# Kernel tuning notes

Measured on AMD Instinct MI355X. Metric: run time of the kernel, lower is better.

## Reference

```python
import jax, jax.numpy as jnp
import numpy as np

D_MODEL = 1024
N_HEADS = 16
HEAD_DIM = D_MODEL // N_HEADS  # 64; used only as softmax scale in windowed path
WINDOW = 128


def _window_starts(seq_len, window):
    # Faithful to the torch loop: stride = window//2, last window right-aligned.
    starts = []
    for i in range(0, seq_len, window // 2):
        end = min(i + window, seq_len)
        starts.append(max(0, end - window))
        if end == seq_len:
            break
    return np.asarray(starts, dtype=np.int32)


def setup_inputs() -> dict:
    key = jax.random.key(0)
    ks = jax.random.split(key, 9)
    B, S = 4, 4096
    sc = 1.0 / np.sqrt(D_MODEL)
    return {
        "x": jax.random.normal(ks[0], (B, S, D_MODEL), jnp.float32),
        "Wq": jax.random.normal(ks[1], (D_MODEL, D_MODEL), jnp.float32) * sc,
        "bq": jax.random.normal(ks[2], (D_MODEL,), jnp.float32) * 0.02,
        "Wk": jax.random.normal(ks[3], (D_MODEL, D_MODEL), jnp.float32) * sc,
        "bk": jax.random.normal(ks[4], (D_MODEL,), jnp.float32) * 0.02,
        "Wv": jax.random.normal(ks[5], (D_MODEL, D_MODEL), jnp.float32) * sc,
        "bv": jax.random.normal(ks[6], (D_MODEL,), jnp.float32) * 0.02,
        "Wo": jax.random.normal(ks[7], (D_MODEL, D_MODEL), jnp.float32) * sc,
        "bo": jax.random.normal(ks[8], (D_MODEL,), jnp.float32) * 0.02,
    }


def reference(x, Wq, bq, Wk, bk, Wv, bv, Wo, bo):
    B, S, D = x.shape
    q = x @ Wq + bq  # [B,S,D]
    k = x @ Wk + bk
    v = x @ Wv + bv

    # Overlapping sliding windows (heads merged, as in the original windowed path).
    starts = _window_starts(S, WINDOW)                      # [W]
    idx = starts[:, None] + np.arange(WINDOW)[None, :]      # [W, w] static
    idx_j = jnp.asarray(idx)
    qw = q[:, idx_j]  # [B, W, w, D]
    kw = k[:, idx_j]
    vw = v[:, idx_j]
    scores = jnp.einsum('bwqd,bwkd->bwqk', qw, kw) / np.sqrt(HEAD_DIM)
    attn = jax.nn.softmax(scores, axis=-1)
    out_w = jnp.einsum('bwqk,bwkd->bwqd', attn, vw)         # [B, W, w, D]

    # Overlap-add then average by coverage counts.
    flat_idx = idx.reshape(-1)
    out = jnp.zeros((B, S, D), x.dtype).at[:, flat_idx].add(
        out_w.reshape(B, -1, D))
    counts = jnp.zeros((S,), x.dtype).at[flat_idx].add(1.0)
    out = out / counts[None, :, None]

    return out @ Wo + bo
```

## Files before the change

kernel.cpp:

```cpp
#include <hip/hip_runtime.h>
#include <stdint.h>
#include <stddef.h>

#define D_MODEL 1024
#define SEQ     4096
#define BATCH   4
#define MTOT    (BATCH*SEQ)
#define NWIN    63

typedef __bf16 bf16;
typedef __bf16 bf16x8 __attribute__((ext_vector_type(8)));
typedef __bf16 bf16x4 __attribute__((ext_vector_type(4)));
typedef float  floatx4 __attribute__((ext_vector_type(4)));

__device__ __forceinline__ void async_ld16(const void* g, void* l) {
  __builtin_amdgcn_global_load_lds(
      (const __attribute__((address_space(1))) unsigned int*)g,
      (__attribute__((address_space(3))) unsigned int*)l,
      16, 0, 0);
}


__global__ __launch_bounds__(256)
void cvt_x_kernel(const float* __restrict__ x, bf16* __restrict__ xb)
{
  const int i = blockIdx.x * 256 + threadIdx.x;
  const float4 v = ((const float4*)x)[i];
  bf16x4 o = { (bf16)v.x, (bf16)v.y, (bf16)v.z, (bf16)v.w };
  ((bf16x4*)xb)[i] = o;
}

__global__ __launch_bounds__(256)
void cvt_wt_kernel(const float* __restrict__ W0, const float* __restrict__ W1,
                   const float* __restrict__ W2, const float* __restrict__ W3,
                   bf16* __restrict__ wt)
{
  __shared__ float tile[32][33];
  const float* Wsel = (blockIdx.z == 0) ? W0 : (blockIdx.z == 1) ? W1
                    : (blockIdx.z == 2) ? W2 : W3;
  bf16* Wt = wt + (size_t)blockIdx.z * D_MODEL * D_MODEL;
  const int tx = threadIdx.x & 31, ty = threadIdx.x >> 5;
  const int tn = blockIdx.x * 32, tk = blockIdx.y * 32;
#pragma unroll
  for (int j = 0; j < 32; j += 8)
    tile[ty + j][tx] = Wsel[(size_t)(tk + ty + j) * D_MODEL + (tn + tx)];
  __syncthreads();
#pragma unroll
  for (int j = 0; j < 32; j += 8)
    Wt[(size_t)(tn + ty + j) * D_MODEL + (tk + tx)] = (bf16)tile[tx][ty + j];
}

__device__ __forceinline__ void gemm_core(const bf16* __restrict__ A,
                                          const bf16* __restrict__ Bt,
                                          int Kdim, int m0, int n0,
                                          bf16* As, bf16* Bs,
                                          floatx4 (&acc)[4][4],
                                          int w, int l)
{
  const int ll = l & 15, lh = l >> 4;
  const int wm = w >> 1, wn = w & 1;

  for (int k0 = 0; k0 < Kdim; k0 += 64) {
#pragma unroll
    for (int i = 0; i < 4; ++i) {
      const int f = w * 4 + i;
      const int mt = f & 7, kk = f >> 3;
      async_ld16(A  + (size_t)(m0 + mt * 16 + ll) * Kdim + (k0 + kk * 32 + lh * 8),
                 &As[f * 512 + l * 8]);
      async_ld16(Bt + (size_t)(n0 + mt * 16 + ll) * Kdim + (k0 + kk * 32 + lh * 8),
                 &Bs[f * 512 + l * 8]);
    }
    __syncthreads();
#pragma unroll
    for (int kk = 0; kk < 2; ++kk) {
      bf16x8 af[4], bfr[4];
#pragma unroll
      for (int t = 0; t < 4; ++t) {
        af[t]  = *(const bf16x8*)&As[(kk * 8 + wm * 4 + t) * 512 + l * 8];
        bfr[t] = *(const bf16x8*)&Bs[(kk * 8 + wn * 4 + t) * 512 + l * 8];
      }
#pragma unroll
      for (int mt = 0; mt < 4; ++mt)
#pragma unroll
        for (int nt = 0; nt < 4; ++nt)
          acc[mt][nt] = __builtin_amdgcn_mfma_f32_16x16x32_bf16(af[mt], bfr[nt], acc[mt][nt], 0, 0, 0);
    }
    __syncthreads();
  }
}

__global__ __launch_bounds__(256)
void gemm_qkv(const bf16* __restrict__ A, const bf16* __restrict__ Bt,
              const float* __restrict__ bq, const float* __restrict__ bk,
              const float* __restrict__ bv,
              bf16* __restrict__ qo, bf16* __restrict__ ko, bf16* __restrict__ vto)
{
  __shared__ __attribute__((aligned(16))) bf16 As[8192];
  __shared__ __attribute__((aligned(16))) bf16 Bs[8192];
  const int tid = threadIdx.x;
  const int w = tid >> 6, l = tid & 63;
  const int ll = l & 15, lh = l >> 4;
  const int wm = w >> 1, wn = w & 1;

  const int idx = blockIdx.x;
  const int xcd = idx & 7;
  const int local = idx >> 3;
  const int msub = local & 3;
  const int nblk = (local >> 2) % 24;
  const int sub  = local / 96;
  const int mblk = xcd * 16 + sub * 4 + msub;
  const int m0 = mblk * 128, n0 = nblk * 128;

  floatx4 acc[4][4];
#pragma unroll
  for (int i = 0; i < 4; ++i)
#pragma unroll
    for (int j = 0; j < 4; ++j) acc[i][j] = (floatx4)0.f;

  gemm_core(A, Bt, D_MODEL, m0, n0, As, Bs, acc, w, l);

  const int sel = n0 >> 10;
  const int ncl = n0 & 1023;
  const float* bias = (sel == 0) ? bq : (sel == 1) ? bk : bv;

#pragma unroll
  for (int mt = 0; mt < 4; ++mt) {
#pragma unroll
    for (int nt = 0; nt < 4; ++nt) {
      const int colL = ncl + wn * 64 + nt * 16 + ll;
      const float bvv = bias[colL];
#pragma unroll
      for (int r = 0; r < 4; ++r) {
        const int row = m0 + wm * 64 + mt * 16 + lh * 4 + r;
        const float v = acc[mt][nt][r] + bvv;
        if (sel == 0) {
          qo[(size_t)row * D_MODEL + colL] = (bf16)v;
        } else if (sel == 1) {
          ko[(size_t)row * D_MODEL + colL] = (bf16)v;
        } else {
          const int bb = row >> 12, s = row & 4095;
          vto[((size_t)bb * D_MODEL + colL) * SEQ + s] = (bf16)v;
        }
      }
    }
  }
}

__global__ __launch_bounds__(256)
void gemm_out(const bf16* __restrict__ A, const bf16* __restrict__ Bt,
              const float* __restrict__ bias, float* __restrict__ C)
{
  __shared__ __attribute__((aligned(16))) bf16 As[8192];
  __shared__ __attribute__((aligned(16))) bf16 Bs[8192];
  const int tid = threadIdx.x;
  const int w = tid >> 6, l = tid & 63;
  const int ll = l & 15, lh = l >> 4;
  const int wm = w >> 1, wn = w & 1;

  const int idx = blockIdx.x;
  const int xcd = idx & 7;
  const int local = idx >> 3;
  const int msub = local & 3;
  const int nblk = (local >> 2) & 7;
  const int sub  = local >> 5;
  const int mblk = xcd * 16 + sub * 4 + msub;
  const int m0 = mblk * 128, n0 = nblk * 128;

  floatx4 acc[4][4];
#pragma unroll
  for (int i = 0; i < 4; ++i)
#pragma unroll
    for (int j = 0; j < 4; ++j) acc[i][j] = (floatx4)0.f;

  gemm_core(A, Bt, D_MODEL, m0, n0, As, Bs, acc, w, l);

#pragma unroll
  for (int mt = 0; mt < 4; ++mt) {
#pragma unroll
    for (int nt = 0; nt < 4; ++nt) {
      const int col = n0 + wn * 64 + nt * 16 + ll;
      const float bvv = bias[col];
#pragma unroll
      for (int r = 0; r < 4; ++r) {
        const int row = m0 + wm * 64 + mt * 16 + lh * 4 + r;
        C[(size_t)row * D_MODEL + col] = acc[mt][nt][r] + bvv;
      }
    }
  }
}

__global__ __launch_bounds__(256)
void qk_softmax(const bf16* __restrict__ qb, const bf16* __restrict__ kb,
                bf16* __restrict__ Pg)
{
  __shared__ __attribute__((aligned(16))) bf16 As[4096];
  __shared__ __attribute__((aligned(16))) bf16 Bs[8192];
  __shared__ float redM[4][64];
  __shared__ float redS[4][64];

  const int tid = threadIdx.x;
  const int w = tid >> 6, l = tid & 63, ll = l & 15, lh = l >> 4;
  const int wh = blockIdx.x;
  const int win = wh >> 1, half = wh & 1;
  const int b = blockIdx.y;

  const bf16* Aq = qb + ((size_t)b * SEQ + win * 64 + half * 64) * D_MODEL;
  const bf16* Ak = kb + ((size_t)b * SEQ + win * 64) * D_MODEL;

  floatx4 acc[4][2];
#pragma unroll
  for (int i = 0; i < 4; ++i)
#pragma unroll
    for (int j = 0; j < 2; ++j) acc[i][j] = (floatx4)0.f;

  for (int c0 = 0; c0 < D_MODEL; c0 += 64) {
#pragma unroll
    for (int i = 0; i < 2; ++i) {
      const int f = w * 2 + i;
      const int mt = f & 3, kk = f >> 2;
      async_ld16(Aq + (size_t)(mt * 16 + ll) * D_MODEL + (c0 + kk * 32 + lh * 8),
                 &As[f * 512 + l * 8]);
    }
#pragma unroll
    for (int i = 0; i < 4; ++i) {
      const int f = w * 4 + i;
      const int mt = f & 7, kk = f >> 3;
      async_ld16(Ak + (size_t)(mt * 16 + ll) * D_MODEL + (c0 + kk * 32 + lh * 8),
                 &Bs[f * 512 + l * 8]);
    }
    __syncthreads();
#pragma unroll
    for (int kk = 0; kk < 2; ++kk) {
      bf16x8 af[4], bfr[2];
#pragma unroll
      for (int t = 0; t < 4; ++t)
        af[t]  = *(const bf16x8*)&As[(kk * 4 + t) * 512 + l * 8];
#pragma unroll
      for (int t = 0; t < 2; ++t)
        bfr[t] = *(const bf16x8*)&Bs[(kk * 8 + w * 2 + t) * 512 + l * 8];
#pragma unroll
      for (int mt = 0; mt < 4; ++mt)
#pragma unroll
        for (int nt = 0; nt < 2; ++nt)
          acc[mt][nt] = __builtin_amdgcn_mfma_f32_16x16x32_bf16(af[mt], bfr[nt], acc[mt][nt], 0, 0, 0);
    }
    __syncthreads();
  }

#pragma unroll
  for (int mt = 0; mt < 4; ++mt)
#pragma unroll
    for (int nt = 0; nt < 2; ++nt)
#pragma unroll
      for (int r = 0; r < 4; ++r) acc[mt][nt][r] *= 0.125f;

#pragma unroll
  for (int mt = 0; mt < 4; ++mt)
#pragma unroll
    for (int r = 0; r < 4; ++r) {
      float m = fmaxf(acc[mt][0][r], acc[mt][1][r]);
      m = fmaxf(m, __shfl_xor(m, 1));
      m = fmaxf(m, __shfl_xor(m, 2));
      m = fmaxf(m, __shfl_xor(m, 4));
      m = fmaxf(m, __shfl_xor(m, 8));
      if (ll == 0) redM[w][mt * 16 + lh * 4 + r] = m;
    }
  __syncthreads();

#pragma unroll
  for (int mt = 0; mt < 4; ++mt)
#pragma unroll
    for (int r = 0; r < 4; ++r) {
      const int row = mt * 16 + lh * 4 + r;
      const float m = fmaxf(fmaxf(redM[0][row], redM[1][row]),
                            fmaxf(redM[2][row], redM[3][row]));
      const float e0 = __expf(acc[mt][0][r] - m);
      const float e1 = __expf(acc[mt][1][r] - m);
      acc[mt][0][r] = e0; acc[mt][1][r] = e1;
      float s = e0 + e1;
      s += __shfl_xor(s, 1);
      s += __shfl_xor(s, 2);
      s += __shfl_xor(s, 4);
      s += __shfl_xor(s, 8);
      if (ll == 0) redS[w][row] = s;
    }
  __syncthreads();

  bf16* Pb = Pg + ((size_t)(b * NWIN + win) * 128 + half * 64) * 128;
#pragma unroll
  for (int mt = 0; mt < 4; ++mt)
#pragma unroll
    for (int r = 0; r < 4; ++r) {
      const int row = mt * 16 + lh * 4 + r;
      const float inv = 1.f / (redS[0][row] + redS[1][row] + redS[2][row] + redS[3][row]);
#pragma unroll
      for (int nt = 0; nt < 2; ++nt)
        Pb[(size_t)row * 128 + w * 32 + nt * 16 + ll] = (bf16)(acc[mt][nt][r] * inv);
    }
}

__global__ __launch_bounds__(256)
void pv_gather(const bf16* __restrict__ Pg, const bf16* __restrict__ vt,
               bf16* __restrict__ ab)
{
  __shared__ __attribute__((aligned(16))) bf16 As[4096];
  __shared__ __attribute__((aligned(16))) bf16 Bs[8192];

  const int tid = threadIdx.x;
  const int w = tid >> 6, l = tid & 63, ll = l & 15, lh = l >> 4;
  const int d0 = blockIdx.x * 128;
  const int h  = blockIdx.y;
  const int b  = blockIdx.z;

  int wseg[2], roff[2];
  int nseg = 0;
  if (h >= 1)        { wseg[nseg] = h - 1; roff[nseg] = 64; ++nseg; }
  if (h <= NWIN - 1) { wseg[nseg] = h;     roff[nseg] = 0;  ++nseg; }
  const float scale = (nseg == 2) ? 0.5f : 1.0f;

  floatx4 acc[4][2];
#pragma unroll
  for (int i = 0; i < 4; ++i)
#pragma unroll
    for (int j = 0; j < 2; ++j) acc[i][j] = (floatx4)0.f;

  for (int sg = 0; sg < nseg; ++sg) {
    const bf16* Pseg = Pg + ((size_t)(b * NWIN + wseg[sg]) * 128 + roff[sg]) * 128;
    const bf16* Vseg = vt + ((size_t)b * D_MODEL + d0) * SEQ + wseg[sg] * 64;
    for (int c0 = 0; c0 < 128; c0 += 64) {
#pragma unroll
      for (int i = 0; i < 2; ++i) {
        const int f = w * 2 + i;
        const int mt = f & 3, kk = f >> 2;
        async_ld16(Pseg + (size_t)(mt * 16 + ll) * 128 + (c0 + kk * 32 + lh * 8),
                   &As[f * 512 + l * 8]);
      }
#pragma unroll
      for (int i = 0; i < 4; ++i) {
        const int f = w * 4 + i;
        const int mt = f & 7, kk = f >> 3;
        async_ld16(Vseg + (size_t)(mt * 16 + ll) * SEQ + (c0 + kk * 32 + lh * 8),
                   &Bs[f * 512 + l * 8]);
      }
      __syncthreads();
#pragma unroll
      for (int kk = 0; kk < 2; ++kk) {
        bf16x8 af[4], bfr[2];
#pragma unroll
        for (int t = 0; t < 4; ++t)
          af[t]  = *(const bf16x8*)&As[(kk * 4 + t) * 512 + l * 8];
#pragma unroll
        for (int t = 0; t < 2; ++t)
          bfr[t] = *(const bf16x8*)&Bs[(kk * 8 + w * 2 + t) * 512 + l * 8];
#pragma unroll
        for (int mt = 0; mt < 4; ++mt)
#pragma unroll
          for (int nt = 0; nt < 2; ++nt)
            acc[mt][nt] = __builtin_amdgcn_mfma_f32_16x16x32_bf16(af[mt], bfr[nt], acc[mt][nt], 0, 0, 0);
      }
      __syncthreads();
    }
  }

#pragma unroll
  for (int mt = 0; mt < 4; ++mt)
#pragma unroll
    for (int nt = 0; nt < 2; ++nt)
#pragma unroll
      for (int r = 0; r < 4; ++r) {
        const int row = h * 64 + mt * 16 + lh * 4 + r;
        const int col = d0 + w * 32 + nt * 16 + ll;
        ab[((size_t)b * SEQ + row) * D_MODEL + col] = (bf16)(acc[mt][nt][r] * scale);
      }
}

extern "C" void kernel_launch(void* const* d_in, const int* in_sizes, int n_in,
                              void* d_out, int out_size, void* d_ws, size_t ws_size,
                              hipStream_t stream)
{
  (void)in_sizes; (void)n_in; (void)out_size;

  const float* x  = (const float*)d_in[0];
  const float* Wq = (const float*)d_in[1];
  const float* bq = (const float*)d_in[2];
  const float* Wk = (const float*)d_in[3];
  const float* bk = (const float*)d_in[4];
  const float* Wv = (const float*)d_in[5];
  const float* bv = (const float*)d_in[6];
  const float* Wo = (const float*)d_in[7];
  const float* bo = (const float*)d_in[8];

  if (ws_size < (size_t)176160768) return;
  char* ws = (char*)d_ws;
  bf16* xb = (bf16*)(ws);
  bf16* pb = (bf16*)(ws);
  bf16* wt = (bf16*)(ws + 33554432);
  bf16* qb = (bf16*)(ws + 41943040);
  bf16* kb = (bf16*)(ws + 75497472);
  bf16* vt = (bf16*)(ws + 109051904);
  bf16* ab = (bf16*)(ws + 142606336);

  cvt_x_kernel<<<16384, 256, 0, stream>>>(x, xb);
  cvt_wt_kernel<<<dim3(32, 32, 4), 256, 0, stream>>>(Wq, Wk, Wv, Wo, wt);

  gemm_qkv<<<3072, 256, 0, stream>>>(xb, wt, bq, bk, bv, qb, kb, vt);

  qk_softmax<<<dim3(126, BATCH), 256, 0, stream>>>(qb, kb, pb);
  pv_gather<<<dim3(8, 64, BATCH), 256, 0, stream>>>(pb, vt, ab);

  gemm_out<<<1024, 256, 0, stream>>>(ab, wt + 3145728, bo, (float*)d_out);
}
```

Before: 497.9 us.

## Double-buffer LDS tiles with register prefetch in GEMM and QK kernels

Replaces the async global-to-LDS loads plus per-iteration sync with a software pipeline. The next K-tile is loaded into registers while MFMAs run on the current LDS buffer, then stored into the alternate buffer. This hides global-load latency behind compute in the QKV, output projection and QK-softmax kernels. In exchange it doubles LDS usage (64KB per block for the GEMMs) and adds register pressure, which may reduce occupancy.

```diff
diff --git a/kernel.cpp b/kernel.cpp
--- a/kernel.cpp
+++ b/kernel.cpp
@@ -50,34 +50,54 @@
     Wt[(size_t)(tn + ty + j) * D_MODEL + (tk + tx)] = (bf16)tile[tx][ty + j];
 }
 
-__device__ __forceinline__ void gemm_core(const bf16* __restrict__ A,
-                                          const bf16* __restrict__ Bt,
-                                          int Kdim, int m0, int n0,
-                                          bf16* As, bf16* Bs,
-                                          floatx4 (&acc)[4][4],
-                                          int w, int l)
+__device__ __forceinline__ void gemm_core_pipe(const bf16* __restrict__ A,
+                                               const bf16* __restrict__ Bt,
+                                               int Kdim, int m0, int n0,
+                                               bf16* As, bf16* Bs,
+                                               floatx4 (&acc)[4][4],
+                                               int w, int l)
 {
   const int ll = l & 15, lh = l >> 4;
   const int wm = w >> 1, wn = w & 1;
 
-  for (int k0 = 0; k0 < Kdim; k0 += 64) {
+  bf16x8 ar[4], br[4];
+
+  auto load_regs = [&](int k0) {
 #pragma unroll
     for (int i = 0; i < 4; ++i) {
       const int f = w * 4 + i;
       const int mt = f & 7, kk = f >> 3;
-      async_ld16(A  + (size_t)(m0 + mt * 16 + ll) * Kdim + (k0 + kk * 32 + lh * 8),
-                 &As[f * 512 + l * 8]);
-      async_ld16(Bt + (size_t)(n0 + mt * 16 + ll) * Kdim + (k0 + kk * 32 + lh * 8),
-                 &Bs[f * 512 + l * 8]);
-    }
-    __syncthreads();
+      ar[i] = *(const bf16x8*)(A  + (size_t)(m0 + mt * 16 + ll) * Kdim + (k0 + kk * 32 + lh * 8));
+      br[i] = *(const bf16x8*)(Bt + (size_t)(n0 + mt * 16 + ll) * Kdim + (k0 + kk * 32 + lh * 8));
+    }
+  };
+  auto store_lds = [&](int buf) {
+    bf16* Ad = As + buf * 8192;
+    bf16* Bd = Bs + buf * 8192;
+#pragma unroll
+    for (int i = 0; i < 4; ++i) {
+      const int f = w * 4 + i;
+      *(bf16x8*)&Ad[f * 512 + l * 8] = ar[i];
+      *(bf16x8*)&Bd[f * 512 + l * 8] = br[i];
+    }
+  };
+
+  load_regs(0);
+  store_lds(0);
+  __syncthreads();
+
+  const int T = Kdim >> 6;
+  for (int t = 0; t < T; ++t) {
+    if (t + 1 < T) load_regs((t + 1) << 6);
+    const bf16* Ac = As + (t & 1) * 8192;
+    const bf16* Bc = Bs + (t & 1) * 8192;
 #pragma unroll
     for (int kk = 0; kk < 2; ++kk) {
       bf16x8 af[4], bfr[4];
 #pragma unroll
-      for (int t = 0; t < 4; ++t) {
-        af[t]  = *(const bf16x8*)&As[(kk * 8 + wm * 4 + t) * 512 + l * 8];
-        bfr[t] = *(const bf16x8*)&Bs[(kk * 8 + wn * 4 + t) * 512 + l * 8];
+      for (int tt = 0; tt < 4; ++tt) {
+        af[tt]  = *(const bf16x8*)&Ac[(kk * 8 + wm * 4 + tt) * 512 + l * 8];
+        bfr[tt] = *(const bf16x8*)&Bc[(kk * 8 + wn * 4 + tt) * 512 + l * 8];
       }
 #pragma unroll
       for (int mt = 0; mt < 4; ++mt)
@@ -85,6 +105,7 @@
         for (int nt = 0; nt < 4; ++nt)
           acc[mt][nt] = __builtin_amdgcn_mfma_f32_16x16x32_bf16(af[mt], bfr[nt], acc[mt][nt], 0, 0, 0);
     }
+    if (t + 1 < T) store_lds((t + 1) & 1);
     __syncthreads();
   }
 }
@@ -95,8 +116,8 @@
               const float* __restrict__ bv,
               bf16* __restrict__ qo, bf16* __restrict__ ko, bf16* __restrict__ vto)
 {
-  __shared__ __attribute__((aligned(16))) bf16 As[8192];
-  __shared__ __attribute__((aligned(16))) bf16 Bs[8192];
+  __shared__ __attribute__((aligned(16))) bf16 As[16384];
+  __shared__ __attribute__((aligned(16))) bf16 Bs[16384];
   const int tid = threadIdx.x;
   const int w = tid >> 6, l = tid & 63;
   const int ll = l & 15, lh = l >> 4;
@@ -117,7 +138,7 @@
 #pragma unroll
     for (int j = 0; j < 4; ++j) acc[i][j] = (floatx4)0.f;
 
-  gemm_core(A, Bt, D_MODEL, m0, n0, As, Bs, acc, w, l);
+  gemm_core_pipe(A, Bt, D_MODEL, m0, n0, As, Bs, acc, w, l);
 
   const int sel = n0 >> 10;
   const int ncl = n0 & 1023;
@@ -150,8 +171,8 @@
 void gemm_out(const bf16* __restrict__ A, const bf16* __restrict__ Bt,
               const float* __restrict__ bias, float* __restrict__ C)
 {
-  __shared__ __attribute__((aligned(16))) bf16 As[8192];
-  __shared__ __attribute__((aligned(16))) bf16 Bs[8192];
+  __shared__ __attribute__((aligned(16))) bf16 As[16384];
+  __shared__ __attribute__((aligned(16))) bf16 Bs[16384];
   const int tid = threadIdx.x;
   const int w = tid >> 6, l = tid & 63;
   const int ll = l & 15, lh = l >> 4;
@@ -172,7 +193,7 @@
 #pragma unroll
     for (int j = 0; j < 4; ++j) acc[i][j] = (floatx4)0.f;
 
-  gemm_core(A, Bt, D_MODEL, m0, n0, As, Bs, acc, w, l);
+  gemm_core_pipe(A, Bt, D_MODEL, m0, n0, As, Bs, acc, w, l);
 
 #pragma unroll
   for (int mt = 0; mt < 4; ++mt) {
@@ -193,8 +214,8 @@
 void qk_softmax(const bf16* __restrict__ qb, const bf16* __restrict__ kb,
                 bf16* __restrict__ Pg)
 {
-  __shared__ __attribute__((aligned(16))) bf16 As[4096];
-  __shared__ __attribute__((aligned(16))) bf16 Bs[8192];
+  __shared__ __attribute__((aligned(16))) bf16 As[8192];
+  __shared__ __attribute__((aligned(16))) bf16 Bs[16384];
   __shared__ float redM[4][64];
   __shared__ float redS[4][64];
 
@@ -213,37 +234,61 @@
 #pragma unroll
     for (int j = 0; j < 2; ++j) acc[i][j] = (floatx4)0.f;
 
-  for (int c0 = 0; c0 < D_MODEL; c0 += 64) {
+  bf16x8 qr[2], kr[4];
+
+  auto load_regs = [&](int c0) {
 #pragma unroll
     for (int i = 0; i < 2; ++i) {
       const int f = w * 2 + i;
       const int mt = f & 3, kk = f >> 2;
-      async_ld16(Aq + (size_t)(mt * 16 + ll) * D_MODEL + (c0 + kk * 32 + lh * 8),
-                 &As[f * 512 + l * 8]);
+      qr[i] = *(const bf16x8*)(Aq + (size_t)(mt * 16 + ll) * D_MODEL + (c0 + kk * 32 + lh * 8));
     }
 #pragma unroll
     for (int i = 0; i < 4; ++i) {
       const int f = w * 4 + i;
       const int mt = f & 7, kk = f >> 3;
-      async_ld16(Ak + (size_t)(mt * 16 + ll) * D_MODEL + (c0 + kk * 32 + lh * 8),
-                 &Bs[f * 512 + l * 8]);
-    }
-    __syncthreads();
+      kr[i] = *(const bf16x8*)(Ak + (size_t)(mt * 16 + ll) * D_MODEL + (c0 + kk * 32 + lh * 8));
+    }
+  };
+  auto store_lds = [&](int buf) {
+    bf16* Ad = As + buf * 4096;
+    bf16* Bd = Bs + buf * 8192;
+#pragma unroll
+    for (int i = 0; i < 2; ++i) {
+      const int f = w * 2 + i;
+      *(bf16x8*)&Ad[f * 512 + l * 8] = qr[i];
+    }
+#pragma unroll
+    for (int i = 0; i < 4; ++i) {
+      const int f = w * 4 + i;
+      *(bf16x8*)&Bd[f * 512 + l * 8] = kr[i];
+    }
+  };
+
+  load_regs(0);
+  store_lds(0);
+  __syncthreads();
+
+  for (int t = 0; t < 16; ++t) {
+    if (t + 1 < 16) load_regs((t + 1) << 6);
+    const bf16* Ac = As + (t & 1) * 4096;
+    const bf16* Bc = Bs + (t & 1) * 8192;
 #pragma unroll
     for (int kk = 0; kk < 2; ++kk) {
       bf16x8 af[4], bfr[2];
 #pragma unroll
-      for (int t = 0; t < 4; ++t)
-        af[t]  = *(const bf16x8*)&As[(kk * 4 + t) * 512 + l * 8];
-#pragma unroll
-      for (int t = 0; t < 2; ++t)
-        bfr[t] = *(const bf16x8*)&Bs[(kk * 8 + w * 2 + t) * 512 + l * 8];
+      for (int tt = 0; tt < 4; ++tt)
+        af[tt]  = *(const bf16x8*)&Ac[(kk * 4 + tt) * 512 + l * 8];
+#pragma unroll
+      for (int tt = 0; tt < 2; ++tt)
+        bfr[tt] = *(const bf16x8*)&Bc[(kk * 8 + w * 2 + tt) * 512 + l * 8];
 #pragma unroll
       for (int mt = 0; mt < 4; ++mt)
 #pragma unroll
         for (int nt = 0; nt < 2; ++nt)
           acc[mt][nt] = __builtin_amdgcn_mfma_f32_16x16x32_bf16(af[mt], bfr[nt], acc[mt][nt], 0, 0, 0);
     }
+    if (t + 1 < 16) store_lds((t + 1) & 1);
     __syncthreads();
   }
 
```

Measured after the change: 496.0 us. No clear change (-0.4%).
